# Kernel tuning notes

Hardware: AMD Instinct MI355X
Metric: run time of the kernel (lower is better)

The kernel has to match this reference:

```python
import jax, jax.numpy as jnp
import numpy as np

B, INPUT_DIM, N = 8, 1, 4096
DIM, DEPTH, HEADS, DIM_HEAD = 512, 4, 8, 64
WINDOW = 128
NUM_CLASSES = 10
INNER = int(DIM * 4 * 2 / 3)  # 1365 (GEGLU FeedForward inner dim)
LN_EPS = 1e-5


def setup_inputs() -> dict:
    key = jax.random.key(0)
    ks = jax.random.split(key, 12)
    s = 0.02
    inner_qkv = HEADS * DIM_HEAD
    return {
        "x": jax.random.normal(ks[0], (B, INPUT_DIM, N), dtype=jnp.float32),
        "lin_emb_w": jax.random.normal(ks[1], (DIM, INPUT_DIM), dtype=jnp.float32) * s,
        "lin_emb_b": jnp.zeros((DIM,), dtype=jnp.float32),
        "qkv_w": jax.random.normal(ks[2], (DEPTH, 3 * inner_qkv, DIM), dtype=jnp.float32) * s,
        "out_w": jax.random.normal(ks[3], (DEPTH, DIM, inner_qkv), dtype=jnp.float32) * s,
        "ff_ln_g": jnp.ones((DEPTH, DIM), dtype=jnp.float32),
        "ff_ln_b": jnp.zeros((DEPTH, DIM), dtype=jnp.float32),
        "ff_w1": jax.random.normal(ks[4], (DEPTH, 2 * INNER, DIM), dtype=jnp.float32) * s,
        "ff_w2": jax.random.normal(ks[5], (DEPTH, DIM, INNER), dtype=jnp.float32) * s,
        "proj_w": jax.random.normal(ks[6], (NUM_CLASSES, DIM), dtype=jnp.float32) * s,
        "proj_b": jnp.zeros((NUM_CLASSES,), dtype=jnp.float32),
    }


def _layer_norm(x, g, b):
    mu = jnp.mean(x, axis=-1, keepdims=True)
    var = jnp.mean(jnp.square(x - mu), axis=-1, keepdims=True)
    return (x - mu) * jax.lax.rsqrt(var + LN_EPS) * g + b


def _local_attention(q, k, v, w):
    # q,k,v: (b, h, n, d). Non-causal sliding window: each window of size w
    # attends to windows [i-1, i, i+1] (look_backward=1, look_forward=1),
    # with out-of-range key positions masked (lucidrains LocalAttention,
    # autopad=True, exact_windowsize=False). n is a multiple of w here.
    b, h, n, d = q.shape
    nw = n // w
    scale = d ** -0.5
    qw = q.reshape(b, h, nw, w, d) * scale
    kw = k.reshape(b, h, nw, w, d)
    vw = v.reshape(b, h, nw, w, d)

    def look_around(t):  # (b,h,nw,w,d) -> (b,h,nw,3w,d)
        tp = jnp.pad(t, ((0, 0), (0, 0), (1, 1), (0, 0), (0, 0)))
        return jnp.concatenate([tp[:, :, i:i + nw] for i in range(3)], axis=3)

    k3 = look_around(kw)
    v3 = look_around(vw)

    # validity mask for boundary windows (fake keys from padding)
    win = jnp.arange(nw)
    kpos = (win[:, None] - 1) * w + jnp.arange(3 * w)[None, :]  # (nw, 3w)
    valid = (kpos >= 0) & (kpos < n)

    scores = jnp.einsum('bhnqd,bhnkd->bhnqk', qw, k3)  # (b,h,nw,w,3w)
    scores = jnp.where(valid[None, None, :, None, :], scores,
                       jnp.finfo(scores.dtype).min)
    attn = jax.nn.softmax(scores, axis=-1)
    out = jnp.einsum('bhnqk,bhnkd->bhnqd', attn, v3)
    return out.reshape(b, h, n, d)


def reference(x, lin_emb_w, lin_emb_b, qkv_w, out_w, ff_ln_g, ff_ln_b,
              ff_w1, ff_w2, proj_w, proj_b):
    b = x.shape[0]
    h = jnp.einsum('bdn,ed->bne', x, lin_emb_w) + lin_emb_b  # (b, n, dim)
    for l in range(DEPTH):
        # --- LocalMHA (no prenorm) + residual ---
        qkv = jnp.einsum('bnd,ed->bne', h, qkv_w[l])
        q, k, v = jnp.split(qkv, 3, axis=-1)
        def heads(t):
            return t.reshape(b, N, HEADS, DIM_HEAD).transpose(0, 2, 1, 3)
        o = _local_attention(heads(q), heads(k), heads(v), WINDOW)
        o = o.transpose(0, 2, 1, 3).reshape(b, N, HEADS * DIM_HEAD)
        h = jnp.einsum('bne,de->bnd', o, out_w[l]) + h
        # --- GEGLU FeedForward (prenorm inside) + residual ---
        y = _layer_norm(h, ff_ln_g[l], ff_ln_b[l])
        y = jnp.einsum('bnd,ed->bne', y, ff_w1[l])
        u, gate = jnp.split(y, 2, axis=-1)
        y = u * jax.nn.gelu(gate, approximate=False)
        h = h + jnp.einsum('bne,de->bnd', y, ff_w2[l])
    pooled = h.mean(axis=1)  # mean_pooling
    return pooled @ proj_w.T + proj_b
```

## Files before the change

### kernel.cpp

```cpp
#include <hip/hip_runtime.h>
#include <hip/hip_bf16.h>
#include <math.h>

typedef __attribute__((ext_vector_type(8))) short short8;
typedef __attribute__((ext_vector_type(4))) float f32x4;

#define MFMA16 __builtin_amdgcn_mfma_f32_16x16x32_bf16

__device__ __forceinline__ short f2bf(float f){
  unsigned u = __float_as_uint(f);
  u = (u + 0x7FFFu + ((u >> 16) & 1u)) >> 16;
  return (short)u;
}

__device__ __forceinline__ float gelu_phi(float g){
  float ax = fabsf(g) * 0.70710678118f;
  float t  = 1.f / (1.f + 0.3275911f * ax);
  float pp = ((((1.061405429f * t - 1.453152027f) * t + 1.421413741f) * t
               - 0.284496736f) * t + 0.254829592f) * t;
  float e  = 1.f - pp * __expf(-ax * ax);
  return 0.5f + copysignf(0.5f, g) * e;
}

__global__ void cast_bf16_kernel(const float* __restrict__ s, short* __restrict__ d, int n){
  int i = blockIdx.x * 256 + threadIdx.x;
  if (i < n) d[i] = f2bf(s[i]);
}

__global__ void w1p_kernel(const float* __restrict__ s, short* __restrict__ d){
  int i = blockIdx.x * 256 + threadIdx.x;
  int c  = i & 511;
  int rl = i >> 9;
  int r  = rl % 2816;
  int l  = rl / 2816;
  int g  = r >> 5, sfx = r & 31;
  int j  = g * 16 + (sfx & 15);
  float v = 0.f;
  if (j < 1365){
    int sr = (sfx < 16) ? j : 1365 + j;
    v = s[((size_t)l * 2730 + sr) * 512 + c];
  }
  d[i] = f2bf(v);
}

__global__ void w2p_kernel(const float* __restrict__ s, short* __restrict__ d){
  int i = blockIdx.x * 256 + threadIdx.x;
  int c = i % 1408;
  int r = i / 1408;
  float v = (c < 1365) ? s[(size_t)r * 1365 + c] : 0.f;
  d[i] = f2bf(v);
}

__global__ void embed_kernel(const float* __restrict__ x, const float* __restrict__ w,
                             const float* __restrict__ bias, float* __restrict__ hf,
                             short* __restrict__ hb){
  long i = ((long)blockIdx.x * 256 + threadIdx.x) * 8;
  long row = i >> 9; int e = (int)(i & 511);
  float xv = x[row];
  float4 w0 = *(const float4*)(w + e),    w1 = *(const float4*)(w + e + 4);
  float4 b0 = *(const float4*)(bias + e), b1 = *(const float4*)(bias + e + 4);
  float4 o0, o1;
  o0.x = xv * w0.x + b0.x; o0.y = xv * w0.y + b0.y;
  o0.z = xv * w0.z + b0.z; o0.w = xv * w0.w + b0.w;
  o1.x = xv * w1.x + b1.x; o1.y = xv * w1.y + b1.y;
  o1.z = xv * w1.z + b1.z; o1.w = xv * w1.w + b1.w;
  *(float4*)(hf + i) = o0; *(float4*)(hf + i + 4) = o1;
  short8 hv;
  hv[0] = f2bf(o0.x); hv[1] = f2bf(o0.y); hv[2] = f2bf(o0.z); hv[3] = f2bf(o0.w);
  hv[4] = f2bf(o1.x); hv[5] = f2bf(o1.y); hv[6] = f2bf(o1.z); hv[7] = f2bf(o1.w);
  *(short8*)(hb + i) = hv;
}

template<int EPI>
__global__ __launch_bounds__(1024, 4)
void gemm256(const short* __restrict__ A, const short* __restrict__ B, int K,
             float* __restrict__ Cres, short* __restrict__ Cbf, int ldcb)
{
  __shared__ short As[4][256][32];
  __shared__ short Bs[4][256][32];
  char* smA = (char*)As;
  char* smB = (char*)Bs;

  const int tid  = threadIdx.x;
  const int lane = tid & 63;
  const int w    = tid >> 6;
  const int wm   = w >> 2;
  const int wn   = w & 3;
  const int NT   = K >> 5;

  const int nwg = gridDim.x * gridDim.y;
  const int f   = blockIdx.y * gridDim.x + blockIdx.x;
  const int sw  = (f & 7) * (nwg >> 3) + (f >> 3);
  const long tm = (long)(sw / gridDim.x) * 256;
  const long tn = (long)(sw % gridDim.x) * 256;

  const int srow = tid >> 2;
  const int sc   = (lane & 3) ^ ((lane >> 3) & 3);
  const short* aS = A + (tm + srow) * (long)K + sc * 8;
  const short* bS = B + (tn + srow) * (long)K + sc * 8;
  const int ldsW = w * 1024;

  auto stgA = [&](int buf, long koff){
    __builtin_amdgcn_global_load_lds((const __attribute__((address_space(1))) void*)(aS + koff),
        (__attribute__((address_space(3))) void*)(smA + buf * 16384 + ldsW), 16, 0, 0);
  };
  auto stgB = [&](int buf, long koff){
    __builtin_amdgcn_global_load_lds((const __attribute__((address_space(1))) void*)(bS + koff),
        (__attribute__((address_space(3))) void*)(smB + buf * 16384 + ldsW), 16, 0, 0);
  };

  f32x4 acc[4][4];
  #pragma unroll
  for (int i = 0; i < 4; i++)
    #pragma unroll
    for (int j = 0; j < 4; j++)
      acc[i][j] = (f32x4){0.f, 0.f, 0.f, 0.f};

  const int rA = wm * 64 + (lane & 15);
  const int rB = wn * 64 + (lane & 15);
  const int abase = rA * 64 + (((lane >> 4) ^ ((rA >> 1) & 3)) * 16);
  const int bbase = rB * 64 + (((lane >> 4) ^ ((rB >> 1) & 3)) * 16);

  stgA(0, 0);  stgB(0, 0);
  stgA(1, 32); stgB(1, 32);
  stgA(2, 64); stgB(2, 64);
  asm volatile("s_waitcnt vmcnt(4)" ::: "memory");
  __builtin_amdgcn_s_barrier();

  for (int t = 0; t < NT; ++t){
    const int cur = (t & 3) * 16384;
    const int stb = (t + 3) & 3;
    const long ko = (long)(t + 3) * 32;
    short8 a0, a1, bb[4];

    #pragma unroll
    for (int ni = 0; ni < 4; ni++)
      bb[ni] = *(const short8*)(smB + cur + bbase + ni * 1024);
    a0 = *(const short8*)(smA + cur + abase);
    a1 = *(const short8*)(smA + cur + abase + 1024);
    if (t + 3 < NT) stgA(stb, ko);
    __builtin_amdgcn_s_barrier();
    asm volatile("s_waitcnt lgkmcnt(0)" ::: "memory");
    __builtin_amdgcn_sched_barrier(0);
    __builtin_amdgcn_s_setprio(1);
    #pragma unroll
    for (int ni = 0; ni < 4; ni++){
      acc[0][ni] = MFMA16(a0, bb[ni], acc[0][ni], 0, 0, 0);
      acc[1][ni] = MFMA16(a1, bb[ni], acc[1][ni], 0, 0, 0);
    }
    __builtin_amdgcn_s_setprio(0);

    a0 = *(const short8*)(smA + cur + abase + 2048);
    a1 = *(const short8*)(smA + cur + abase + 3072);
    if (t + 3 < NT) stgB(stb, ko);
    __builtin_amdgcn_s_barrier();
    asm volatile("s_waitcnt lgkmcnt(0)" ::: "memory");
    __builtin_amdgcn_sched_barrier(0);
    __builtin_amdgcn_s_setprio(1);
    #pragma unroll
    for (int ni = 0; ni < 4; ni++){
      acc[2][ni] = MFMA16(a0, bb[ni], acc[2][ni], 0, 0, 0);
      acc[3][ni] = MFMA16(a1, bb[ni], acc[3][ni], 0, 0, 0);
    }
    __builtin_amdgcn_s_setprio(0);
    if      (t + 3 < NT) asm volatile("s_waitcnt vmcnt(4)" ::: "memory");
    else if (t + 2 < NT) asm volatile("s_waitcnt vmcnt(2)" ::: "memory");
    else if (t + 1 < NT) asm volatile("s_waitcnt vmcnt(0)" ::: "memory");
    __builtin_amdgcn_s_barrier();
  }

  #pragma unroll
  for (int mi = 0; mi < 4; mi++){
    if (EPI == 3){
      #pragma unroll
      for (int p = 0; p < 2; p++){
        #pragma unroll
        for (int v = 0; v < 4; v++){
          long row = tm + wm * 64 + mi * 16 + (lane >> 4) * 4 + v;
          long col = (tn >> 1) + wn * 32 + p * 16 + (lane & 15);
          float u = acc[mi][2 * p][v];
          float g = acc[mi][2 * p + 1][v];
          Cbf[row * ldcb + col] = f2bf(u * g * gelu_phi(g));
        }
      }
    } else {
      #pragma unroll
      for (int ni = 0; ni < 4; ni++){
        #pragma unroll
        for (int v = 0; v < 4; v++){
          long row = tm + wm * 64 + mi * 16 + (lane >> 4) * 4 + v;
          long col = tn + wn * 64 + ni * 16 + (lane & 15);
          float x = acc[mi][ni][v];
          if (EPI == 0){
            Cbf[row * ldcb + col] = f2bf(x);
          } else if (EPI == 1){
            Cres[row * 512 + col] = x + Cres[row * 512 + col];
          } else {
            float rr = x + Cres[row * 512 + col];
            Cres[row * 512 + col] = rr;
            Cbf[row * 512 + col] = f2bf(rr);
          }
        }
      }
    }
  }
}

__global__ __launch_bounds__(256, 2)
void attn_kernel(const short* __restrict__ qkv, short* __restrict__ o)
{
  __shared__ short Ks[128 * 64];
  __shared__ short Vt[64 * 136];
  __shared__ short Ps[4 * 32 * 128];
  const int win = blockIdx.x, hh = blockIdx.y, b = blockIdx.z;
  const int tid = threadIdx.x, lane = tid & 63, w = tid >> 6;
  const long qrow0 = (long)b * 4096 + (long)win * 128;

  short8 qf[2][2];
  #pragma unroll
  for (int i = 0; i < 2; i++)
    #pragma unroll
    for (int kk = 0; kk < 2; kk++)
      qf[i][kk] = *(const short8*)(qkv + (qrow0 + w * 32 + i * 16 + (lane & 15)) * 1536
                                   + hh * 64 + kk * 32 + (lane >> 4) * 8);

  f32x4 oacc[2][4];
  #pragma unroll
  for (int i = 0; i < 2; i++)
    #pragma unroll
    for (int j = 0; j < 4; j++)
      oacc[i][j] = (f32x4){0.f, 0.f, 0.f, 0.f};
  float rs[2][4];
  #pragma unroll
  for (int i = 0; i < 2; i++)
    #pragma unroll
    for (int v = 0; v < 4; v++)
      rs[i][v] = 0.f;

  const int row_s = tid >> 3, c_s = tid & 7;
  for (int cc = 0; cc < 3; cc++){
    int kw = win - 1 + cc;
    if (kw < 0 || kw >= 32) continue;
    const long krow0 = (long)b * 4096 + (long)kw * 128;
    __syncthreads();
    #pragma unroll
    for (int r = 0; r < 4; r++){
      int row = row_s + r * 32;
      const short* src = qkv + (krow0 + row) * 1536 + hh * 64;
      short8 kv = *(const short8*)(src + 512 + c_s * 8);
      *(short8*)((char*)Ks + ((row * 128 + c_s * 16) ^ ((row & 7) << 4))) = kv;
      short8 vv = *(const short8*)(src + 1024 + c_s * 8);
      #pragma unroll
      for (int e = 0; e < 8; e++) Vt[(c_s * 8 + e) * 136 + row] = vv[e];
    }
    __syncthreads();

    f32x4 sacc[2][8];
    #pragma unroll
    for (int i = 0; i < 2; i++)
      #pragma unroll
      for (int j = 0; j < 8; j++)
        sacc[i][j] = (f32x4){0.f, 0.f, 0.f, 0.f};
    #pragma unroll
    for (int kk = 0; kk < 2; kk++){
      short8 bbk[8];
      int ac = (kk * 32 + (lane >> 4) * 8) * 2;
      #pragma unroll
      for (int j = 0; j < 8; j++){
        int br = j * 16 + (lane & 15);
        bbk[j] = *(const short8*)((char*)Ks + ((br * 128 + ac) ^ ((br & 7) << 4)));
      }
      #pragma unroll
      for (int i = 0; i < 2; i++)
        #pragma unroll
        for (int j = 0; j < 8; j++)
          sacc[i][j] = MFMA16(qf[i][kk], bbk[j], sacc[i][j], 0, 0, 0);
    }

    short* myPs = Ps + w * 32 * 128;
    float psum[2][4];
    #pragma unroll
    for (int i = 0; i < 2; i++)
      #pragma unroll
      for (int v = 0; v < 4; v++)
        psum[i][v] = 0.f;
    #pragma unroll
    for (int i = 0; i < 2; i++)
      #pragma unroll
      for (int j = 0; j < 8; j++)
        #pragma unroll
        for (int v = 0; v < 4; v++){
          float p = expf(0.125f * sacc[i][j][v]);
          psum[i][v] += p;
          int prow = i * 16 + (lane >> 4) * 4 + v;
          int pcb  = (j * 16 + (lane & 15)) * 2;
          *(short*)((char*)myPs + ((prow * 256 + pcb) ^ ((prow & 7) << 4))) = f2bf(p);
        }
    #pragma unroll
    for (int i = 0; i < 2; i++)
      #pragma unroll
      for (int v = 0; v < 4; v++){
        float s = psum[i][v];
        s += __shfl_xor(s, 1); s += __shfl_xor(s, 2);
        s += __shfl_xor(s, 4); s += __shfl_xor(s, 8);
        rs[i][v] += s;
      }
    __syncthreads();

    #pragma unroll
    for (int kk = 0; kk < 4; kk++){
      short8 pa[2], vb[4];
      int kb = (kk * 32 + (lane >> 4) * 8) * 2;
      #pragma unroll
      for (int i = 0; i < 2; i++){
        int pr = i * 16 + (lane & 15);
        pa[i] = *(const short8*)((char*)myPs + ((pr * 256 + kb) ^ ((pr & 7) << 4)));
      }
      #pragma unroll
      for (int j = 0; j < 4; j++){
        int vr = j * 16 + (lane & 15);
        vb[j] = *(const short8*)((char*)Vt + (vr * 272 + kb));
      }
      #pragma unroll
      for (int i = 0; i < 2; i++)
        #pragma unroll
        for (int j = 0; j < 4; j++)
          oacc[i][j] = MFMA16(pa[i], vb[j], oacc[i][j], 0, 0, 0);
    }
  }

  #pragma unroll
  for (int i = 0; i < 2; i++)
    #pragma unroll
    for (int j = 0; j < 4; j++)
      #pragma unroll
      for (int v = 0; v < 4; v++){
        long row = qrow0 + w * 32 + i * 16 + (lane >> 4) * 4 + v;
        int col = hh * 64 + j * 16 + (lane & 15);
        o[row * 512 + col] = f2bf(oacc[i][j][v] / rs[i][v]);
      }
}

__global__ __launch_bounds__(256)
void ln_kernel(const float* __restrict__ h, const float* __restrict__ g,
               const float* __restrict__ be, short* __restrict__ y)
{
  long row = (long)blockIdx.x * 4 + (threadIdx.x >> 6);
  int lane = threadIdx.x & 63;
  const float* x = h + row * 512 + lane * 8;
  float4 a0 = *(const float4*)x;
  float4 a1 = *(const float4*)(x + 4);
  float v[8] = {a0.x, a0.y, a0.z, a0.w, a1.x, a1.y, a1.z, a1.w};
  float s = 0.f, sq = 0.f;
  #pragma unroll
  for (int j = 0; j < 8; j++){ s += v[j]; sq += v[j] * v[j]; }
  #pragma unroll
  for (int m = 1; m <= 32; m <<= 1){ s += __shfl_xor(s, m); sq += __shfl_xor(sq, m); }
  float mu = s * (1.f / 512.f);
  float var = sq * (1.f / 512.f) - mu * mu;
  float rstd = rsqrtf(var + 1e-5f);
  short* yo = y + row * 512 + lane * 8;
  #pragma unroll
  for (int j = 0; j < 8; j++){
    int c = lane * 8 + j;
    yo[j] = f2bf((v[j] - mu) * rstd * g[c] + be[c]);
  }
}

__global__ void pool_partial(const float* __restrict__ h, float* __restrict__ part){
  int b = blockIdx.x, ch = blockIdx.y, t = threadIdx.x;
  float s0 = 0.f, s1 = 0.f;
  const float* base = h + ((long)b * 4096 + ch * 128) * 512;
  for (int n = 0; n < 128; n++){
    s0 += base[(long)n * 512 + t];
    s1 += base[(long)n * 512 + t + 256];
  }
  part[((b * 32 + ch) * 512) + t] = s0;
  part[((b * 32 + ch) * 512) + t + 256] = s1;
}

__global__ void pool_proj(const float* __restrict__ part, const float* __restrict__ pw,
                          const float* __restrict__ pb, float* __restrict__ out){
  __shared__ float pooled[512];
  __shared__ float red[4];
  int b = blockIdx.x, t = threadIdx.x;
  int lane = t & 63, w = t >> 6;
  float s0 = 0.f, s1 = 0.f;
  for (int ch = 0; ch < 32; ch++){
    s0 += part[((b * 32 + ch) * 512) + t];
    s1 += part[((b * 32 + ch) * 512) + t + 256];
  }
  pooled[t] = s0 * (1.f / 4096.f);
  pooled[t + 256] = s1 * (1.f / 4096.f);
  __syncthreads();
  for (int cls = 0; cls < 10; cls++){
    float p = pooled[t] * pw[cls * 512 + t] + pooled[t + 256] * pw[cls * 512 + t + 256];
    p += __shfl_xor(p, 1); p += __shfl_xor(p, 2); p += __shfl_xor(p, 4);
    p += __shfl_xor(p, 8); p += __shfl_xor(p, 16); p += __shfl_xor(p, 32);
    if (lane == 0) red[w] = p;
    __syncthreads();
    if (t == 0) out[b * 10 + cls] = red[0] + red[1] + red[2] + red[3] + pb[cls];
    __syncthreads();
  }
}

extern "C" void kernel_launch(void* const* d_in, const int* in_sizes, int n_in,
                              void* d_out, int out_size, void* d_ws, size_t ws_size,
                              hipStream_t stream)
{
  const float* x      = (const float*)d_in[0];
  const float* lin_w  = (const float*)d_in[1];
  const float* lin_b  = (const float*)d_in[2];
  const float* qkvw_f = (const float*)d_in[3];
  const float* outw_f = (const float*)d_in[4];
  const float* lng    = (const float*)d_in[5];
  const float* lnb    = (const float*)d_in[6];
  const float* w1_f   = (const float*)d_in[7];
  const float* w2_f   = (const float*)d_in[8];
  const float* projw  = (const float*)d_in[9];
  const float* projb  = (const float*)d_in[10];
  float* out = (float*)d_out;

  char* ws = (char*)d_ws;
  float* hf32 = (float*)(ws);
  short* abuf = (short*)(ws + 67108864);
  short* qkvb = (short*)(ws + 100663296);
  short* gbuf = qkvb;
  short* obuf = (short*)(ws + 201326592);
  float* part = (float*)(ws + 234881024);
  short* wqkv = (short*)(ws + 235405312);
  short* wout = (short*)(ws + 247988224);
  short* w1p  = (short*)(ws + 250085376);
  short* w2p  = (short*)(ws + 261619712);

  cast_bf16_kernel<<<12288, 256, 0, stream>>>(qkvw_f, wqkv, 4 * 1536 * 512);
  cast_bf16_kernel<<<4096, 256, 0, stream>>>(outw_f, wout, 4 * 512 * 512);
  w1p_kernel<<<22528, 256, 0, stream>>>(w1_f, w1p);
  w2p_kernel<<<11264, 256, 0, stream>>>(w2_f, w2p);
  embed_kernel<<<8192, 256, 0, stream>>>(x, lin_w, lin_b, hf32, abuf);

  for (int l = 0; l < 4; l++){
    gemm256<0><<<dim3(6, 128), 1024, 0, stream>>>(abuf, wqkv + (size_t)l * 1536 * 512, 512,
                                                  nullptr, qkvb, 1536);
    attn_kernel<<<dim3(32, 8, 8), 256, 0, stream>>>(qkvb, obuf);
    gemm256<1><<<dim3(2, 128), 1024, 0, stream>>>(obuf, wout + (size_t)l * 512 * 512, 512,
                                                  hf32, nullptr, 0);
    ln_kernel<<<8192, 256, 0, stream>>>(hf32, lng + l * 512, lnb + l * 512, abuf);
    gemm256<3><<<dim3(11, 128), 1024, 0, stream>>>(abuf, w1p + (size_t)l * 2816 * 512, 512,
                                                   nullptr, gbuf, 1408);
    gemm256<2><<<dim3(2, 128), 1024, 0, stream>>>(gbuf, w2p + (size_t)l * 512 * 1408, 1408,
                                                  hf32, abuf, 512);
  }
  pool_partial<<<dim3(8, 32), 256, 0, stream>>>(hf32, part);
  pool_proj<<<8, 256, 0, stream>>>(part, projw, projb, out);
}
```

Baseline: 1.816 ms.

## Store GEMM operands in 256x32 tile-packed layout and merge the k-step barriers

Weights and activations feeding the GEMMs (embed, LN, attention output, GEGLU output, residual bf16 copy) are now written in a tile-packed layout: 256-row by 32-column blocks stored contiguously. Each global-to-LDS load then reads one contiguous 16 KB chunk instead of strided rows. The GEMM main loop also issues both A and B prefetches at the top and does all 16 MFMAs after a single LDS wait, dropping the intermediate barrier. The change costs more registers for the A fragments and scatters the epilogue stores. It relies on every producer and consumer agreeing on the packed indexing, and the attention kernel's reads of qkvb are left row-major.

Result: slower. 1.904 ms (median of 2 runs) (+4.8%).

```diff
diff --git a/kernel.cpp b/kernel.cpp
--- a/kernel.cpp
+++ b/kernel.cpp
@@ -6,11 +6,18 @@
 typedef __attribute__((ext_vector_type(4))) float f32x4;
 
 #define MFMA16 __builtin_amdgcn_mfma_f32_16x16x32_bf16
+#define GLOAD(dst, src) __builtin_amdgcn_global_load_lds( \
+    (const __attribute__((address_space(1))) void*)(src), \
+    (__attribute__((address_space(3))) void*)(dst), 16, 0, 0)
 
 __device__ __forceinline__ short f2bf(float f){
   unsigned u = __float_as_uint(f);
   u = (u + 0x7FFFu + ((u >> 16) & 1u)) >> 16;
   return (short)u;
+}
+
+__device__ __forceinline__ size_t pidx(int r, int k, int K){
+  return ((size_t)((r >> 8) * (K >> 5) + (k >> 5)) * 256 + (r & 255)) * 32 + (k & 31);
 }
 
 __device__ __forceinline__ float gelu_phi(float g){
@@ -22,9 +29,13 @@
   return 0.5f + copysignf(0.5f, g) * e;
 }
 
-__global__ void cast_bf16_kernel(const float* __restrict__ s, short* __restrict__ d, int n){
+__global__ void cast_pack_kernel(const float* __restrict__ s, short* __restrict__ d,
+                                 int NROW, int K){
   int i = blockIdx.x * 256 + threadIdx.x;
-  if (i < n) d[i] = f2bf(s[i]);
+  int per = NROW * K;
+  int l = i / per, rem = i - l * per;
+  int r = rem / K, c = rem - r * K;
+  d[(size_t)l * per + pidx(r, c, K)] = f2bf(s[i]);
 }
 
 __global__ void w1p_kernel(const float* __restrict__ s, short* __restrict__ d){
@@ -40,15 +51,16 @@
     int sr = (sfx < 16) ? j : 1365 + j;
     v = s[((size_t)l * 2730 + sr) * 512 + c];
   }
-  d[i] = f2bf(v);
+  d[(size_t)l * 2816 * 512 + pidx(r, c, 512)] = f2bf(v);
 }
 
 __global__ void w2p_kernel(const float* __restrict__ s, short* __restrict__ d){
   int i = blockIdx.x * 256 + threadIdx.x;
   int c = i % 1408;
-  int r = i / 1408;
-  float v = (c < 1365) ? s[(size_t)r * 1365 + c] : 0.f;
-  d[i] = f2bf(v);
+  int rr = i / 1408;
+  int l = rr >> 9, row = rr & 511;
+  float v = (c < 1365) ? s[(size_t)rr * 1365 + c] : 0.f;
+  d[(size_t)l * 512 * 1408 + pidx(row, c, 1408)] = f2bf(v);
 }
 
 __global__ void embed_kernel(const float* __restrict__ x, const float* __restrict__ w,
@@ -60,108 +72,75 @@
   float4 w0 = *(const float4*)(w + e),    w1 = *(const float4*)(w + e + 4);
   float4 b0 = *(const float4*)(bias + e), b1 = *(const float4*)(bias + e + 4);
   float4 o0, o1;
-  o0.x = xv * w0.x + b0.x; o0.y = xv * w0.y + b0.y;
-  o0.z = xv * w0.z + b0.z; o0.w = xv * w0.w + b0.w;
-  o1.x = xv * w1.x + b1.x; o1.y = xv * w1.y + b1.y;
-  o1.z = xv * w1.z + b1.z; o1.w = xv * w1.w + b1.w;
+  o0.x = xv*w0.x+b0.x; o0.y = xv*w0.y+b0.y; o0.z = xv*w0.z+b0.z; o0.w = xv*w0.w+b0.w;
+  o1.x = xv*w1.x+b1.x; o1.y = xv*w1.y+b1.y; o1.z = xv*w1.z+b1.z; o1.w = xv*w1.w+b1.w;
   *(float4*)(hf + i) = o0; *(float4*)(hf + i + 4) = o1;
   short8 hv;
-  hv[0] = f2bf(o0.x); hv[1] = f2bf(o0.y); hv[2] = f2bf(o0.z); hv[3] = f2bf(o0.w);
-  hv[4] = f2bf(o1.x); hv[5] = f2bf(o1.y); hv[6] = f2bf(o1.z); hv[7] = f2bf(o1.w);
-  *(short8*)(hb + i) = hv;
+  hv[0]=f2bf(o0.x); hv[1]=f2bf(o0.y); hv[2]=f2bf(o0.z); hv[3]=f2bf(o0.w);
+  hv[4]=f2bf(o1.x); hv[5]=f2bf(o1.y); hv[6]=f2bf(o1.z); hv[7]=f2bf(o1.w);
+  *(short8*)(hb + pidx((int)row, e, 512)) = hv;
 }
 
 template<int EPI>
 __global__ __launch_bounds__(1024, 4)
-void gemm256(const short* __restrict__ A, const short* __restrict__ B, int K,
+void gemm_pk(const short* __restrict__ A, const short* __restrict__ B, int K,
              float* __restrict__ Cres, short* __restrict__ Cbf, int ldcb)
 {
   __shared__ short As[4][256][32];
   __shared__ short Bs[4][256][32];
-  char* smA = (char*)As;
-  char* smB = (char*)Bs;
-
-  const int tid  = threadIdx.x;
-  const int lane = tid & 63;
-  const int w    = tid >> 6;
-  const int wm   = w >> 2;
-  const int wn   = w & 3;
-  const int NT   = K >> 5;
-
+  char* smA = (char*)As; char* smB = (char*)Bs;
+  const int tid = threadIdx.x, lane = tid & 63, w = tid >> 6;
+  const int wm = w >> 2, wn = w & 3;
+  const int NT = K >> 5;
   const int nwg = gridDim.x * gridDim.y;
-  const int f   = blockIdx.y * gridDim.x + blockIdx.x;
-  const int sw  = (f & 7) * (nwg >> 3) + (f >> 3);
+  const int f = blockIdx.y * gridDim.x + blockIdx.x;
+  const int sw = (f & 7) * (nwg >> 3) + (f >> 3);
   const long tm = (long)(sw / gridDim.x) * 256;
   const long tn = (long)(sw % gridDim.x) * 256;
 
   const int srow = tid >> 2;
-  const int sc   = (lane & 3) ^ ((lane >> 3) & 3);
-  const short* aS = A + (tm + srow) * (long)K + sc * 8;
-  const short* bS = B + (tn + srow) * (long)K + sc * 8;
+  const int sc   = (tid & 3) ^ ((srow >> 1) & 3);
+  const short* aS = A + ((size_t)(tm >> 8) * NT * 256 + srow) * 32 + sc * 8;
+  const short* bS = B + ((size_t)(tn >> 8) * NT * 256 + srow) * 32 + sc * 8;
   const int ldsW = w * 1024;
 
-  auto stgA = [&](int buf, long koff){
-    __builtin_amdgcn_global_load_lds((const __attribute__((address_space(1))) void*)(aS + koff),
-        (__attribute__((address_space(3))) void*)(smA + buf * 16384 + ldsW), 16, 0, 0);
-  };
-  auto stgB = [&](int buf, long koff){
-    __builtin_amdgcn_global_load_lds((const __attribute__((address_space(1))) void*)(bS + koff),
-        (__attribute__((address_space(3))) void*)(smB + buf * 16384 + ldsW), 16, 0, 0);
-  };
-
   f32x4 acc[4][4];
   #pragma unroll
   for (int i = 0; i < 4; i++)
     #pragma unroll
-    for (int j = 0; j < 4; j++)
-      acc[i][j] = (f32x4){0.f, 0.f, 0.f, 0.f};
+    for (int j = 0; j < 4; j++) acc[i][j] = (f32x4){0.f,0.f,0.f,0.f};
 
   const int rA = wm * 64 + (lane & 15);
   const int rB = wn * 64 + (lane & 15);
   const int abase = rA * 64 + (((lane >> 4) ^ ((rA >> 1) & 3)) * 16);
   const int bbase = rB * 64 + (((lane >> 4) ^ ((rB >> 1) & 3)) * 16);
 
-  stgA(0, 0);  stgB(0, 0);
-  stgA(1, 32); stgB(1, 32);
-  stgA(2, 64); stgB(2, 64);
+  GLOAD(smA + 0 + ldsW, aS);           GLOAD(smB + 0 + ldsW, bS);
+  GLOAD(smA + 16384 + ldsW, aS + 8192);  GLOAD(smB + 16384 + ldsW, bS + 8192);
+  GLOAD(smA + 32768 + ldsW, aS + 16384); GLOAD(smB + 32768 + ldsW, bS + 16384);
   asm volatile("s_waitcnt vmcnt(4)" ::: "memory");
   __builtin_amdgcn_s_barrier();
 
   for (int t = 0; t < NT; ++t){
     const int cur = (t & 3) * 16384;
-    const int stb = (t + 3) & 3;
-    const long ko = (long)(t + 3) * 32;
-    short8 a0, a1, bb[4];
-
+    const int stb = ((t + 3) & 3) * 16384;
+    const size_t ko = (size_t)(t + 3) * 8192;
+    if (t + 3 < NT){ GLOAD(smA + stb + ldsW, aS + ko); GLOAD(smB + stb + ldsW, bS + ko); }
+    short8 a[4], bb[4];
     #pragma unroll
     for (int ni = 0; ni < 4; ni++)
       bb[ni] = *(const short8*)(smB + cur + bbase + ni * 1024);
-    a0 = *(const short8*)(smA + cur + abase);
-    a1 = *(const short8*)(smA + cur + abase + 1024);
-    if (t + 3 < NT) stgA(stb, ko);
-    __builtin_amdgcn_s_barrier();
+    #pragma unroll
+    for (int q = 0; q < 4; q++)
+      a[q] = *(const short8*)(smA + cur + abase + q * 1024);
     asm volatile("s_waitcnt lgkmcnt(0)" ::: "memory");
     __builtin_amdgcn_sched_barrier(0);
     __builtin_amdgcn_s_setprio(1);
     #pragma unroll
-    for (int ni = 0; ni < 4; ni++){
-      acc[0][ni] = MFMA16(a0, bb[ni], acc[0][ni], 0, 0, 0);
-      acc[1][ni] = MFMA16(a1, bb[ni], acc[1][ni], 0, 0, 0);
-    }
-    __builtin_amdgcn_s_setprio(0);
-
-    a0 = *(const short8*)(smA + cur + abase + 2048);
-    a1 = *(const short8*)(smA + cur + abase + 3072);
-    if (t + 3 < NT) stgB(stb, ko);
-    __builtin_amdgcn_s_barrier();
-    asm volatile("s_waitcnt lgkmcnt(0)" ::: "memory");
-    __builtin_amdgcn_sched_barrier(0);
-    __builtin_amdgcn_s_setprio(1);
-    #pragma unroll
-    for (int ni = 0; ni < 4; ni++){
-      acc[2][ni] = MFMA16(a0, bb[ni], acc[2][ni], 0, 0, 0);
-      acc[3][ni] = MFMA16(a1, bb[ni], acc[3][ni], 0, 0, 0);
-    }
+    for (int q = 0; q < 4; q++)
+      #pragma unroll
+      for (int ni = 0; ni < 4; ni++)
+        acc[q][ni] = MFMA16(a[q], bb[ni], acc[q][ni], 0, 0, 0);
     __builtin_amdgcn_s_setprio(0);
     if      (t + 3 < NT) asm volatile("s_waitcnt vmcnt(4)" ::: "memory");
     else if (t + 2 < NT) asm volatile("s_waitcnt vmcnt(2)" ::: "memory");
@@ -173,35 +152,28 @@
   for (int mi = 0; mi < 4; mi++){
     if (EPI == 3){
       #pragma unroll
-      for (int p = 0; p < 2; p++){
+      for (int p = 0; p < 2; p++)
         #pragma unroll
         for (int v = 0; v < 4; v++){
-          long row = tm + wm * 64 + mi * 16 + (lane >> 4) * 4 + v;
-          long col = (tn >> 1) + wn * 32 + p * 16 + (lane & 15);
-          float u = acc[mi][2 * p][v];
-          float g = acc[mi][2 * p + 1][v];
-          Cbf[row * ldcb + col] = f2bf(u * g * gelu_phi(g));
+          int row = (int)(tm + wm * 64 + mi * 16 + (lane >> 4) * 4 + v);
+          int col = (int)((tn >> 1) + wn * 32 + p * 16 + (lane & 15));
+          float u = acc[mi][2*p][v], g = acc[mi][2*p+1][v];
+          Cbf[pidx(row, col, 1408)] = f2bf(u * g * gelu_phi(g));
         }
-      }
     } else {
       #pragma unroll
-      for (int ni = 0; ni < 4; ni++){
+      for (int ni = 0; ni < 4; ni++)
         #pragma unroll
         for (int v = 0; v < 4; v++){
-          long row = tm + wm * 64 + mi * 16 + (lane >> 4) * 4 + v;
-          long col = tn + wn * 64 + ni * 16 + (lane & 15);
+          int row = (int)(tm + wm * 64 + mi * 16 + (lane >> 4) * 4 + v);
+          int col = (int)(tn + wn * 64 + ni * 16 + (lane & 15));
           float x = acc[mi][ni][v];
-          if (EPI == 0){
-            Cbf[row * ldcb + col] = f2bf(x);
-          } else if (EPI == 1){
-            Cres[row * 512 + col] = x + Cres[row * 512 + col];
-          } else {
-            float rr = x + Cres[row * 512 + col];
-            Cres[row * 512 + col] = rr;
-            Cbf[row * 512 + col] = f2bf(rr);
-          }
+          if (EPI == 0) Cbf[(long)row * ldcb + col] = f2bf(x);
+          else if (EPI == 1) Cres[(long)row * 512 + col] = x + Cres[(long)row * 512 + col];
+          else { float rr = x + Cres[(long)row * 512 + col];
+                 Cres[(long)row * 512 + col] = rr;
+                 Cbf[pidx(row, col, 512)] = f2bf(rr); }
         }
-      }
     }
   }
 }
@@ -228,14 +200,12 @@
   #pragma unroll
   for (int i = 0; i < 2; i++)
     #pragma unroll
-    for (int j = 0; j < 4; j++)
-      oacc[i][j] = (f32x4){0.f, 0.f, 0.f, 0.f};
+    for (int j = 0; j < 4; j++) oacc[i][j] = (f32x4){0.f,0.f,0.f,0.f};
   float rs[2][4];
   #pragma unroll
   for (int i = 0; i < 2; i++)
     #pragma unroll
-    for (int v = 0; v < 4; v++)
-      rs[i][v] = 0.f;
+    for (int v = 0; v < 4; v++) rs[i][v] = 0.f;
 
   const int row_s = tid >> 3, c_s = tid & 7;
   for (int cc = 0; cc < 3; cc++){
@@ -259,8 +229,7 @@
     #pragma unroll
     for (int i = 0; i < 2; i++)
       #pragma unroll
-      for (int j = 0; j < 8; j++)
-        sacc[i][j] = (f32x4){0.f, 0.f, 0.f, 0.f};
+      for (int j = 0; j < 8; j++) sacc[i][j] = (f32x4){0.f,0.f,0.f,0.f};
     #pragma unroll
     for (int kk = 0; kk < 2; kk++){
       short8 bbk[8];
@@ -282,8 +251,7 @@
     #pragma unroll
     for (int i = 0; i < 2; i++)
       #pragma unroll
-      for (int v = 0; v < 4; v++)
-        psum[i][v] = 0.f;
+      for (int v = 0; v < 4; v++) psum[i][v] = 0.f;
     #pragma unroll
     for (int i = 0; i < 2; i++)
       #pragma unroll
@@ -335,9 +303,9 @@
     for (int j = 0; j < 4; j++)
       #pragma unroll
       for (int v = 0; v < 4; v++){
-        long row = qrow0 + w * 32 + i * 16 + (lane >> 4) * 4 + v;
+        int row = (int)(qrow0 + w * 32 + i * 16 + (lane >> 4) * 4 + v);
         int col = hh * 64 + j * 16 + (lane & 15);
-        o[row * 512 + col] = f2bf(oacc[i][j][v] / rs[i][v]);
+        o[pidx(row, col, 512)] = f2bf(oacc[i][j][v] / rs[i][v]);
       }
 }
 
@@ -359,12 +327,13 @@
   float mu = s * (1.f / 512.f);
   float var = sq * (1.f / 512.f) - mu * mu;
   float rstd = rsqrtf(var + 1e-5f);
-  short* yo = y + row * 512 + lane * 8;
+  short8 yv;
   #pragma unroll
   for (int j = 0; j < 8; j++){
     int c = lane * 8 + j;
-    yo[j] = f2bf((v[j] - mu) * rstd * g[c] + be[c]);
-  }
+    yv[j] = f2bf((v[j] - mu) * rstd * g[c] + be[c]);
+  }
+  *(short8*)(y + pidx((int)row, lane * 8, 512)) = yv;
 }
 
 __global__ void pool_partial(const float* __restrict__ h, float* __restrict__ part){
@@ -433,22 +402,22 @@
   short* w1p  = (short*)(ws + 250085376);
   short* w2p  = (short*)(ws + 261619712);
 
-  cast_bf16_kernel<<<12288, 256, 0, stream>>>(qkvw_f, wqkv, 4 * 1536 * 512);
-  cast_bf16_kernel<<<4096, 256, 0, stream>>>(outw_f, wout, 4 * 512 * 512);
+  cast_pack_kernel<<<12288, 256, 0, stream>>>(qkvw_f, wqkv, 1536, 512);
+  cast_pack_kernel<<<4096, 256, 0, stream>>>(outw_f, wout, 512, 512);
   w1p_kernel<<<22528, 256, 0, stream>>>(w1_f, w1p);
   w2p_kernel<<<11264, 256, 0, stream>>>(w2_f, w2p);
   embed_kernel<<<8192, 256, 0, stream>>>(x, lin_w, lin_b, hf32, abuf);
 
   for (int l = 0; l < 4; l++){
-    gemm256<0><<<dim3(6, 128), 1024, 0, stream>>>(abuf, wqkv + (size_t)l * 1536 * 512, 512,
+    gemm_pk<0><<<dim3(6, 128), 1024, 0, stream>>>(abuf, wqkv + (size_t)l * 1536 * 512, 512,
                                                   nullptr, qkvb, 1536);
     attn_kernel<<<dim3(32, 8, 8), 256, 0, stream>>>(qkvb, obuf);
-    gemm256<1><<<dim3(2, 128), 1024, 0, stream>>>(obuf, wout + (size_t)l * 512 * 512, 512,
+    gemm_pk<1><<<dim3(2, 128), 1024, 0, stream>>>(obuf, wout + (size_t)l * 512 * 512, 512,
                                                   hf32, nullptr, 0);
     ln_kernel<<<8192, 256, 0, stream>>>(hf32, lng + l * 512, lnb + l * 512, abuf);
-    gemm256<3><<<dim3(11, 128), 1024, 0, stream>>>(abuf, w1p + (size_t)l * 2816 * 512, 512,
+    gemm_pk<3><<<dim3(11, 128), 1024, 0, stream>>>(abuf, w1p + (size_t)l * 2816 * 512, 512,
                                                    nullptr, gbuf, 1408);
-    gemm256<2><<<dim3(2, 128), 1024, 0, stream>>>(gbuf, w2p + (size_t)l * 512 * 1408, 1408,
+    gemm_pk<2><<<dim3(2, 128), 1024, 0, stream>>>(gbuf, w2p + (size_t)l * 512 * 1408, 1408,
                                                   hf32, abuf, 512);
   }
   pool_partial<<<dim3(8, 32), 256, 0, stream>>>(hf32, part);
```
